# Kernel tuning notes

Measured on AMD Instinct MI355X. Metric: run time of the kernel, lower is better.

The kernel has to match this reference:

```python
import jax, jax.numpy as jnp
import numpy as np

OUT, IN, BLK, RANK = 4096, 4096, 32, 16
N_BLOCKS = IN // BLK  # 128
Q_ZERO = 128.0  # center of unsigned code range, maps codes to signed values


def setup_inputs() -> dict:
    key = jax.random.key(0)
    ks = jax.random.split(key, 6)
    x = jax.random.normal(ks[0], (4, 2048, IN), dtype=jnp.float32)
    # GGML-style block-quantized weight: int codes in blocks of 32 + per-block fp scale
    q_weight = jax.random.randint(ks[1], (OUT, N_BLOCKS, BLK), 0, 256, dtype=jnp.int32)
    scales = jax.random.uniform(ks[2], (OUT, N_BLOCKS), dtype=jnp.float32) * 0.02
    # LoRA patch applied to dequantized weight
    lora_up = jax.random.normal(ks[3], (OUT, RANK), dtype=jnp.float32) * 0.02
    lora_down = jax.random.normal(ks[4], (RANK, IN), dtype=jnp.float32) * 0.02
    bias = jax.random.normal(ks[5], (OUT,), dtype=jnp.float32)
    return {"x": x, "q_weight": q_weight, "scales": scales,
            "lora_up": lora_up, "lora_down": lora_down, "bias": bias}


def reference(x, q_weight, scales, lora_up, lora_down, bias):
    # 1) dequantize: per-block scale * centered int codes -> full fp weight [OUT, IN]
    w = (q_weight.astype(jnp.float32) - Q_ZERO) * scales[:, :, None]
    w = w.reshape(OUT, IN)
    # 2) apply LoRA patch to the dequantized weight (patch function in get_weight)
    w = w + lora_up @ lora_down
    # 3) delegate to the linear forward operation: y = x @ W^T + b
    return jnp.einsum('bsd,od->bso', x, w) + bias
```

## Files before the change

kernel.cpp:

```cpp
#include <hip/hip_runtime.h>
#include <cstdint>
#include <cstddef>

#define M_TOT 8192
#define N_TOT 4096
#define K_TOT 4096
#define RANK  16

#define BM 256
#define BN 256
#define BK 64
#define NT (K_TOT / BK)

typedef float f32x4 __attribute__((ext_vector_type(4)));
typedef __bf16 bf16x8 __attribute__((ext_vector_type(8)));
typedef unsigned short u16x8 __attribute__((ext_vector_type(8)));

__device__ __forceinline__ unsigned short f32_to_bf16(float f) {
    union { float f; uint32_t u; } v; v.f = f;
    uint32_t r = v.u + (0x7fffu + ((v.u >> 16) & 1u));
    return (unsigned short)(r >> 16);
}

__device__ __forceinline__ void gload_lds16(const void* g, void* l) {
    __builtin_amdgcn_global_load_lds(
        (const __attribute__((address_space(1))) void*)g,
        (__attribute__((address_space(3))) void*)l,
        16, 0, 0);
}

__global__ __launch_bounds__(256) void convert_x_kernel(const float* __restrict__ x,
                                                        unsigned short* __restrict__ xb,
                                                        int n8) {
    int i = blockIdx.x * 256 + threadIdx.x;
    if (i >= n8) return;
    float4 a = ((const float4*)x)[2 * (size_t)i];
    float4 b = ((const float4*)x)[2 * (size_t)i + 1];
    u16x8 o;
    o[0] = f32_to_bf16(a.x); o[1] = f32_to_bf16(a.y);
    o[2] = f32_to_bf16(a.z); o[3] = f32_to_bf16(a.w);
    o[4] = f32_to_bf16(b.x); o[5] = f32_to_bf16(b.y);
    o[6] = f32_to_bf16(b.z); o[7] = f32_to_bf16(b.w);
    *(u16x8*)&xb[(size_t)i * 8] = o;
}

__global__ __launch_bounds__(256) void build_w_kernel(const int* __restrict__ q,
                                                      const float* __restrict__ scales,
                                                      const float* __restrict__ up,
                                                      const float* __restrict__ down,
                                                      unsigned short* __restrict__ W) {
    const int o0 = blockIdx.x * 4;
    const int t = threadIdx.x;
    __shared__ float u[4][RANK];
    if (t < 64) u[t >> 4][t & 15] = up[(o0 + (t >> 4)) * RANK + (t & 15)];
    __syncthreads();

#pragma unroll
    for (int cc = 0; cc < 2; cc++) {
        const int c = t + 256 * cc;
        const int k0 = c * 8;
        float acc[4][8];
#pragma unroll
        for (int row = 0; row < 4; row++) {
            const int o = o0 + row;
            int4 qa = *(const int4*)&q[(size_t)o * K_TOT + k0];
            int4 qb = *(const int4*)&q[(size_t)o * K_TOT + k0 + 4];
            const float s = scales[o * (K_TOT / 32) + (k0 >> 5)];
            acc[row][0] = (float)(qa.x - 128) * s;
            acc[row][1] = (float)(qa.y - 128) * s;
            acc[row][2] = (float)(qa.z - 128) * s;
            acc[row][3] = (float)(qa.w - 128) * s;
            acc[row][4] = (float)(qb.x - 128) * s;
            acc[row][5] = (float)(qb.y - 128) * s;
            acc[row][6] = (float)(qb.z - 128) * s;
            acc[row][7] = (float)(qb.w - 128) * s;
        }
#pragma unroll
        for (int r = 0; r < RANK; r++) {
            float4 da = *(const float4*)&down[r * K_TOT + k0];
            float4 db = *(const float4*)&down[r * K_TOT + k0 + 4];
#pragma unroll
            for (int row = 0; row < 4; row++) {
                const float ur = u[row][r];
                acc[row][0] += ur * da.x; acc[row][1] += ur * da.y;
                acc[row][2] += ur * da.z; acc[row][3] += ur * da.w;
                acc[row][4] += ur * db.x; acc[row][5] += ur * db.y;
                acc[row][6] += ur * db.z; acc[row][7] += ur * db.w;
            }
        }
#pragma unroll
        for (int row = 0; row < 4; row++) {
            u16x8 o8;
#pragma unroll
            for (int j = 0; j < 8; j++) o8[j] = f32_to_bf16(acc[row][j]);
            *(u16x8*)&W[(size_t)(o0 + row) * K_TOT + k0] = o8;
        }
    }
}

#define BARRIER() do { asm volatile("" ::: "memory"); \
                       __builtin_amdgcn_s_barrier(); \
                       asm volatile("" ::: "memory"); } while (0)

__global__ __launch_bounds__(512, 2) void gemm_bt_kernel(const unsigned short* __restrict__ A,
                                                         const unsigned short* __restrict__ B,
                                                         const float* __restrict__ bias,
                                                         float* __restrict__ C) {
    __shared__ unsigned short As[2][2][128 * BK];
    __shared__ unsigned short Bs[2][2][128 * BK];

    const int tid  = (int)threadIdx.x;
    const int wave = tid >> 6;
    const int lane = tid & 63;
    const int wm   = wave >> 2;
    const int wn   = wave & 3;
    const int wbh  = wn >> 1;
    const int wbr  = (wn & 1) * 64;

    int lin = (int)(blockIdx.y * gridDim.x + blockIdx.x);
    lin = (lin & 7) * 64 + (lin >> 3);
    const int tile_n = (lin & 15) * BN;
    const int tile_m = (lin >> 4) * BM;

    const int srow  = tid >> 3;
    const int sk    = ((tid & 7) ^ (srow & 7)) * 8;
    const int wbase = wave * 512;

    const int l16  = lane & 15;
    const int quad = lane >> 4;
    const int sw   = l16 & 7;
    const int slot0 = ((quad ^ sw) * 8);
    const int slot1 = (((4 + quad) ^ sw) * 8);

    const unsigned short* aBase = A + (size_t)(tile_m + srow) * K_TOT + sk;
    const unsigned short* bBase = B + (size_t)(tile_n + srow) * K_TOT + sk;

#define STAGE_A(d, h, t) do { \
    gload_lds16(aBase + (size_t)((h) * 128) * K_TOT + (size_t)(t) * BK, &As[d][h][wbase]); \
    gload_lds16(aBase + (size_t)((h) * 128 + 64) * K_TOT + (size_t)(t) * BK, &As[d][h][4096 + wbase]); \
  } while (0)
#define STAGE_B(d, h, t) do { \
    gload_lds16(bBase + (size_t)((h) * 128) * K_TOT + (size_t)(t) * BK, &Bs[d][h][wbase]); \
    gload_lds16(bBase + (size_t)((h) * 128 + 64) * K_TOT + (size_t)(t) * BK, &Bs[d][h][4096 + wbase]); \
  } while (0)

    f32x4 acc[8][4];
#pragma unroll
    for (int i = 0; i < 8; i++)
#pragma unroll
        for (int j = 0; j < 4; j++) { f32x4 z = {0.f, 0.f, 0.f, 0.f}; acc[i][j] = z; }

    STAGE_A(0, 0, 0); STAGE_A(0, 1, 0);
    STAGE_B(0, 0, 0); STAGE_B(0, 1, 0);
    STAGE_A(1, 0, 1); STAGE_A(1, 1, 1);
    asm volatile("s_waitcnt vmcnt(4)" ::: "memory");
    BARRIER();

    for (int t = 0; t < NT; ++t) {
        const int cur = t & 1, nxt = cur ^ 1;
        const unsigned short* Ah = &As[cur][wm][l16 * BK];
        const unsigned short* Bh = &Bs[cur][wbh][(wbr + l16) * BK];

        bf16x8 af[4][2], bfA[2][2], bfB[2][2];

        if (t + 1 < NT) STAGE_B(nxt, 0, t + 1);
#pragma unroll
        for (int mi = 0; mi < 4; mi++) {
            af[mi][0] = *(const bf16x8*)&Ah[(mi * 16) * BK + slot0];
            af[mi][1] = *(const bf16x8*)&Ah[(mi * 16) * BK + slot1];
        }
#pragma unroll
        for (int ni = 0; ni < 2; ni++) {
            bfA[ni][0] = *(const bf16x8*)&Bh[(ni * 16) * BK + slot0];
            bfA[ni][1] = *(const bf16x8*)&Bh[(ni * 16) * BK + slot1];
        }
        BARRIER();
        __builtin_amdgcn_s_setprio(1);
#pragma unroll
        for (int mi = 0; mi < 4; mi++)
#pragma unroll
            for (int ni = 0; ni < 2; ni++) {
                acc[mi][ni] = __builtin_amdgcn_mfma_f32_16x16x32_bf16(af[mi][0], bfA[ni][0], acc[mi][ni], 0, 0, 0);
                acc[mi][ni] = __builtin_amdgcn_mfma_f32_16x16x32_bf16(af[mi][1], bfA[ni][1], acc[mi][ni], 0, 0, 0);
            }
        __builtin_amdgcn_s_setprio(0);
        BARRIER();

        if (t + 1 < NT) STAGE_B(nxt, 1, t + 1);
#pragma unroll
        for (int ni = 0; ni < 2; ni++) {
            bfB[ni][0] = *(const bf16x8*)&Bh[((ni + 2) * 16) * BK + slot0];
            bfB[ni][1] = *(const bf16x8*)&Bh[((ni + 2) * 16) * BK + slot1];
        }
        BARRIER();
        __builtin_amdgcn_s_setprio(1);
#pragma unroll
        for (int mi = 0; mi < 4; mi++)
#pragma unroll
            for (int ni = 0; ni < 2; ni++) {
                acc[mi][ni + 2] = __builtin_amdgcn_mfma_f32_16x16x32_bf16(af[mi][0], bfB[ni][0], acc[mi][ni + 2], 0, 0, 0);
                acc[mi][ni + 2] = __builtin_amdgcn_mfma_f32_16x16x32_bf16(af[mi][1], bfB[ni][1], acc[mi][ni + 2], 0, 0, 0);
            }
        __builtin_amdgcn_s_setprio(0);
        BARRIER();

#pragma unroll
        for (int mi = 0; mi < 4; mi++) {
            af[mi][0] = *(const bf16x8*)&Ah[((mi + 4) * 16) * BK + slot0];
            af[mi][1] = *(const bf16x8*)&Ah[((mi + 4) * 16) * BK + slot1];
        }
        BARRIER();
        __builtin_amdgcn_s_setprio(1);
#pragma unroll
        for (int mi = 0; mi < 4; mi++)
#pragma unroll
            for (int ni = 0; ni < 2; ni++) {
                acc[mi + 4][ni + 2] = __builtin_amdgcn_mfma_f32_16x16x32_bf16(af[mi][0], bfB[ni][0], acc[mi + 4][ni + 2], 0, 0, 0);
                acc[mi + 4][ni + 2] = __builtin_amdgcn_mfma_f32_16x16x32_bf16(af[mi][1], bfB[ni][1], acc[mi + 4][ni + 2], 0, 0, 0);
            }
        __builtin_amdgcn_s_setprio(0);
        BARRIER();

        if (t + 2 < NT) { STAGE_A(cur, 0, t + 2); STAGE_A(cur, 1, t + 2); }
        __builtin_amdgcn_s_setprio(1);
#pragma unroll
        for (int mi = 0; mi < 4; mi++)
#pragma unroll
            for (int ni = 0; ni < 2; ni++) {
                acc[mi + 4][ni] = __builtin_amdgcn_mfma_f32_16x16x32_bf16(af[mi][0], bfA[ni][0], acc[mi + 4][ni], 0, 0, 0);
                acc[mi + 4][ni] = __builtin_amdgcn_mfma_f32_16x16x32_bf16(af[mi][1], bfA[ni][1], acc[mi + 4][ni], 0, 0, 0);
            }
        __builtin_amdgcn_s_setprio(0);
        if (t + 1 < NT) {
            if (t + 2 < NT) asm volatile("s_waitcnt vmcnt(4)" ::: "memory");
            else            asm volatile("s_waitcnt vmcnt(0)" ::: "memory");
        }
        BARRIER();
    }

#pragma unroll
    for (int ni = 0; ni < 4; ni++) {
        const int col = tile_n + wn * 64 + ni * 16 + l16;
        const float bv = bias[col];
#pragma unroll
        for (int mi = 0; mi < 8; mi++) {
#pragma unroll
            for (int r = 0; r < 4; r++) {
                const int row = tile_m + wm * 128 + mi * 16 + quad * 4 + r;
                C[(size_t)row * N_TOT + col] = acc[mi][ni][r] + bv;
            }
        }
    }
#undef STAGE_A
#undef STAGE_B
}

extern "C" void kernel_launch(void* const* d_in, const int* in_sizes, int n_in,
                              void* d_out, int out_size, void* d_ws, size_t ws_size,
                              hipStream_t stream) {
    const float* x      = (const float*)d_in[0];
    const int*   q      = (const int*)d_in[1];
    const float* scales = (const float*)d_in[2];
    const float* up     = (const float*)d_in[3];
    const float* down   = (const float*)d_in[4];
    const float* bias   = (const float*)d_in[5];
    float* out = (float*)d_out;

    unsigned short* xb = (unsigned short*)d_ws;
    unsigned short* wb = xb + (size_t)M_TOT * K_TOT;

    const int n8 = M_TOT * K_TOT / 8;
    convert_x_kernel<<<n8 / 256, 256, 0, stream>>>(x, xb, n8);
    build_w_kernel<<<N_TOT / 4, 256, 0, stream>>>(q, scales, up, down, wb);
    gemm_bt_kernel<<<dim3(N_TOT / BN, M_TOT / BM), 512, 0, stream>>>(xb, wb, bias, out);
}
```

Measured before the change: 614.3 us.

## Reorganize MFMA phases by k-half with explicit LDS waits and sched barriers

Restructures the per-tile inner schedule so each of four phases handles one k-slot (slot0/slot1) across all four N sub-tiles, rather than splitting by N halves with both k-slots. Register fragments are reorganized (bA/bB per k-slot, a single aF reused), which cuts live fragment registers. Explicit lgkmcnt(0) waits and sched_barrier fences pin the order of LDS reads and MFMAs, stopping the compiler from interleaving them. The B-tile staging now has to happen after the slot0 B fragments are read, and the fixed ordering may leave less room to hide LDS latency.

```diff
diff --git a/kernel.cpp b/kernel.cpp
--- a/kernel.cpp
+++ b/kernel.cpp
@@ -101,6 +101,8 @@
 #define BARRIER() do { asm volatile("" ::: "memory"); \
                        __builtin_amdgcn_s_barrier(); \
                        asm volatile("" ::: "memory"); } while (0)
+#define WAITL0()  asm volatile("s_waitcnt lgkmcnt(0)" ::: "memory")
+#define SCHED0()  __builtin_amdgcn_sched_barrier(0)
 
 __global__ __launch_bounds__(512, 2) void gemm_bt_kernel(const unsigned short* __restrict__ A,
                                                          const unsigned short* __restrict__ B,
@@ -158,79 +160,76 @@
 
     for (int t = 0; t < NT; ++t) {
         const int cur = t & 1, nxt = cur ^ 1;
-        const unsigned short* Ah = &As[cur][wm][l16 * BK];
-        const unsigned short* Bh = &Bs[cur][wbh][(wbr + l16) * BK];
-
-        bf16x8 af[4][2], bfA[2][2], bfB[2][2];
+        const unsigned short* __restrict__ Ah = &As[cur][wm][l16 * BK];
+        const unsigned short* __restrict__ Bh = &Bs[cur][wbh][(wbr + l16) * BK];
+
+        bf16x8 bA[4], bB[4], aF[4];
 
         if (t + 1 < NT) STAGE_B(nxt, 0, t + 1);
 #pragma unroll
-        for (int mi = 0; mi < 4; mi++) {
-            af[mi][0] = *(const bf16x8*)&Ah[(mi * 16) * BK + slot0];
-            af[mi][1] = *(const bf16x8*)&Ah[(mi * 16) * BK + slot1];
-        }
-#pragma unroll
-        for (int ni = 0; ni < 2; ni++) {
-            bfA[ni][0] = *(const bf16x8*)&Bh[(ni * 16) * BK + slot0];
-            bfA[ni][1] = *(const bf16x8*)&Bh[(ni * 16) * BK + slot1];
-        }
-        BARRIER();
-        __builtin_amdgcn_s_setprio(1);
-#pragma unroll
-        for (int mi = 0; mi < 4; mi++)
-#pragma unroll
-            for (int ni = 0; ni < 2; ni++) {
-                acc[mi][ni] = __builtin_amdgcn_mfma_f32_16x16x32_bf16(af[mi][0], bfA[ni][0], acc[mi][ni], 0, 0, 0);
-                acc[mi][ni] = __builtin_amdgcn_mfma_f32_16x16x32_bf16(af[mi][1], bfA[ni][1], acc[mi][ni], 0, 0, 0);
-            }
-        __builtin_amdgcn_s_setprio(0);
+        for (int ni = 0; ni < 4; ni++) bA[ni] = *(const bf16x8*)&Bh[(ni * 16) * BK + slot0];
+#pragma unroll
+        for (int mi = 0; mi < 4; mi++) aF[mi] = *(const bf16x8*)&Ah[(mi * 16) * BK + slot0];
+        BARRIER();
+        WAITL0();
+        SCHED0();
+        __builtin_amdgcn_s_setprio(1);
+#pragma unroll
+        for (int mi = 0; mi < 4; mi++)
+#pragma unroll
+            for (int ni = 0; ni < 4; ni++)
+                acc[mi][ni] = __builtin_amdgcn_mfma_f32_16x16x32_bf16(aF[mi], bA[ni], acc[mi][ni], 0, 0, 0);
+        __builtin_amdgcn_s_setprio(0);
+        SCHED0();
         BARRIER();
 
         if (t + 1 < NT) STAGE_B(nxt, 1, t + 1);
 #pragma unroll
-        for (int ni = 0; ni < 2; ni++) {
-            bfB[ni][0] = *(const bf16x8*)&Bh[((ni + 2) * 16) * BK + slot0];
-            bfB[ni][1] = *(const bf16x8*)&Bh[((ni + 2) * 16) * BK + slot1];
-        }
-        BARRIER();
-        __builtin_amdgcn_s_setprio(1);
-#pragma unroll
-        for (int mi = 0; mi < 4; mi++)
-#pragma unroll
-            for (int ni = 0; ni < 2; ni++) {
-                acc[mi][ni + 2] = __builtin_amdgcn_mfma_f32_16x16x32_bf16(af[mi][0], bfB[ni][0], acc[mi][ni + 2], 0, 0, 0);
-                acc[mi][ni + 2] = __builtin_amdgcn_mfma_f32_16x16x32_bf16(af[mi][1], bfB[ni][1], acc[mi][ni + 2], 0, 0, 0);
-            }
-        __builtin_amdgcn_s_setprio(0);
-        BARRIER();
-
-#pragma unroll
-        for (int mi = 0; mi < 4; mi++) {
-            af[mi][0] = *(const bf16x8*)&Ah[((mi + 4) * 16) * BK + slot0];
-            af[mi][1] = *(const bf16x8*)&Ah[((mi + 4) * 16) * BK + slot1];
-        }
-        BARRIER();
-        __builtin_amdgcn_s_setprio(1);
-#pragma unroll
-        for (int mi = 0; mi < 4; mi++)
-#pragma unroll
-            for (int ni = 0; ni < 2; ni++) {
-                acc[mi + 4][ni + 2] = __builtin_amdgcn_mfma_f32_16x16x32_bf16(af[mi][0], bfB[ni][0], acc[mi + 4][ni + 2], 0, 0, 0);
-                acc[mi + 4][ni + 2] = __builtin_amdgcn_mfma_f32_16x16x32_bf16(af[mi][1], bfB[ni][1], acc[mi + 4][ni + 2], 0, 0, 0);
-            }
-        __builtin_amdgcn_s_setprio(0);
-        BARRIER();
-
+        for (int ni = 0; ni < 4; ni++) bB[ni] = *(const bf16x8*)&Bh[(ni * 16) * BK + slot1];
+#pragma unroll
+        for (int mi = 0; mi < 4; mi++) aF[mi] = *(const bf16x8*)&Ah[(mi * 16) * BK + slot1];
+        BARRIER();
+        WAITL0();
+        SCHED0();
+        __builtin_amdgcn_s_setprio(1);
+#pragma unroll
+        for (int mi = 0; mi < 4; mi++)
+#pragma unroll
+            for (int ni = 0; ni < 4; ni++)
+                acc[mi][ni] = __builtin_amdgcn_mfma_f32_16x16x32_bf16(aF[mi], bB[ni], acc[mi][ni], 0, 0, 0);
+        __builtin_amdgcn_s_setprio(0);
+        SCHED0();
+        BARRIER();
+
+#pragma unroll
+        for (int mi = 0; mi < 4; mi++) aF[mi] = *(const bf16x8*)&Ah[((mi + 4) * 16) * BK + slot0];
+        BARRIER();
+        WAITL0();
+        SCHED0();
+        __builtin_amdgcn_s_setprio(1);
+#pragma unroll
+        for (int mi = 0; mi < 4; mi++)
+#pragma unroll
+            for (int ni = 0; ni < 4; ni++)
+                acc[mi + 4][ni] = __builtin_amdgcn_mfma_f32_16x16x32_bf16(aF[mi], bA[ni], acc[mi + 4][ni], 0, 0, 0);
+        __builtin_amdgcn_s_setprio(0);
+        SCHED0();
+        BARRIER();
+
+#pragma unroll
+        for (int mi = 0; mi < 4; mi++) aF[mi] = *(const bf16x8*)&Ah[((mi + 4) * 16) * BK + slot1];
+        BARRIER();
         if (t + 2 < NT) { STAGE_A(cur, 0, t + 2); STAGE_A(cur, 1, t + 2); }
-        __builtin_amdgcn_s_setprio(1);
-#pragma unroll
-        for (int mi = 0; mi < 4; mi++)
-#pragma unroll
-            for (int ni = 0; ni < 2; ni++) {
-                acc[mi + 4][ni] = __builtin_amdgcn_mfma_f32_16x16x32_bf16(af[mi][0], bfA[ni][0], acc[mi + 4][ni], 0, 0, 0);
-                acc[mi + 4][ni] = __builtin_amdgcn_mfma_f32_16x16x32_bf16(af[mi][1], bfA[ni][1], acc[mi + 4][ni], 0, 0, 0);
-            }
-        __builtin_amdgcn_s_setprio(0);
+        WAITL0();
+        SCHED0();
+        __builtin_amdgcn_s_setprio(1);
+#pragma unroll
+        for (int mi = 0; mi < 4; mi++)
+#pragma unroll
+            for (int ni = 0; ni < 4; ni++)
+                acc[mi + 4][ni] = __builtin_amdgcn_mfma_f32_16x16x32_bf16(aF[mi], bB[ni], acc[mi + 4][ni], 0, 0, 0);
+        __builtin_amdgcn_s_setprio(0);
+        SCHED0();
         if (t + 1 < NT) {
             if (t + 2 < NT) asm volatile("s_waitcnt vmcnt(4)" ::: "memory");
             else            asm volatile("s_waitcnt vmcnt(0)" ::: "memory");
```

Measured after the change: 598.0 us. 1.03x faster.
